# Kernel optimization log

Hardware: AMD Instinct MI355X
Metric: run time of the kernel (lower is better)

Reference implementation:

```python
import jax, jax.numpy as jnp
import numpy as np

# DeepSeek-style MLA decode paged attention (vLLM HPU flat_pa_mla, latent cache path)
B = 32              # batch (decode requests)
H = 16              # q heads (TP shard)
KV_LORA = 512       # kv_lora_rank
ROPE = 64           # qk_rope_head_dim
D = KV_LORA + ROPE  # 576, latent+rope dim
BS = 128            # block_size
BLOCKS_PER_SEQ = 16 # 2048-token context
NB = B * BLOCKS_PER_SEQ   # 512 active blocks
NCACHE = 1024       # blocks in the paged cache
SCALE = 192 ** -0.5  # 1/sqrt(qk_nope(128)+rope(64))
NEG = -1.0e9


def setup_inputs() -> dict:
    key = jax.random.key(0)
    k1, k2, k3, k4 = jax.random.split(key, 4)
    query = jax.random.normal(k1, (B, H, D), dtype=jnp.float32)
    key_cache = jax.random.normal(k2, (NCACHE, BS, D), dtype=jnp.float32)
    # each active block points at some cache block
    block_list = jax.random.randint(k3, (NB,), 0, NCACHE, dtype=jnp.int32)
    # contiguous grouping: blocks_per_seq blocks per request
    block_groups = jnp.repeat(jnp.arange(B, dtype=jnp.int32), BLOCKS_PER_SEQ)
    block_mapping = jax.nn.one_hot(block_groups, B, dtype=jnp.float32)  # [NB, B]
    # per-block usage in [1, BS]; unused tail positions masked out
    usage = jax.random.randint(k4, (NB,), 1, BS + 1)
    block_bias = jnp.where(jnp.arange(BS)[None, :] < usage[:, None], 0.0, NEG).astype(jnp.float32)
    return {"query": query, "key_cache": key_cache, "block_mapping": block_mapping,
            "block_bias": block_bias, "block_list": block_list, "block_groups": block_groups}


def reference(query, key_cache, block_mapping, block_bias, block_list, block_groups):
    # batch2block: scatter per-batch query to its blocks via one-hot matmul
    q = SCALE * jnp.einsum('nb,bhd->nhd', block_mapping, query)      # [NB,H,D]
    kv = key_cache[block_list]                                       # [NB,BS,D] fetched latent KV
    v = kv[..., :KV_LORA]                                            # [NB,BS,V]
    attn = jnp.einsum('nhd,nsd->nhs', q, kv) + block_bias[:, None, :]  # [NB,H,BS]
    # per-block online softmax pieces
    block_max = attn.max(axis=-1, keepdims=True)                     # [NB,H,1]
    p = jnp.exp(attn - block_max)
    block_sums = p.sum(axis=-1)                                      # [NB,H]
    o = jnp.einsum('nhs,nsv->nhv', p, v)                             # [NB,H,V]
    bm = block_max[..., 0]                                           # [NB,H]
    # grouped max over blocks of the same request, broadcast back to blocks
    group_max = jax.ops.segment_max(bm, block_groups, num_segments=B)[block_groups]
    adj = jnp.exp(bm - group_max)                                    # [NB,H]
    sum_adj = block_sums * adj
    # block2batch then batch2block of the adjusted sums
    group_sum = jnp.einsum('nb,nh->bh', block_mapping, sum_adj)
    group_sum = jnp.einsum('nb,bh->nh', block_mapping, group_sum)
    group_sum = jnp.maximum(group_sum, sum_adj)
    rescale = adj / group_sum
    o = o * rescale[..., None]
    # block2batch: sum rescaled partial outputs per request
    out = jnp.einsum('nb,nhv->bhv', block_mapping, o)                # [B,H,V]
    return out
```

## Files before the change

### kernel.cpp

```cpp
#include <hip/hip_runtime.h>
#include <math.h>

#define NB_ 512
#define B_ 32
#define H_ 16
#define D_ 576
#define KV_ 512
#define BS_ 128
#define SCALE_ 0.07216878364870323f

typedef __attribute__((ext_vector_type(8))) short bf16x8;
typedef __attribute__((ext_vector_type(4))) float f32x4;

__device__ float g_o[NB_ * H_ * KV_];
__device__ float g_bm[NB_ * H_];
__device__ float g_bs[NB_ * H_];

typedef const __attribute__((address_space(1))) void* gp_t;
typedef __attribute__((address_space(3))) void* lp_t;
typedef __attribute__((address_space(3))) char* l3p;

static __device__ __forceinline__ void glds16(const float* g, l3p l) {
    __builtin_amdgcn_global_load_lds((gp_t)g, (lp_t)l, 16, 0, 0);
}

static __device__ __forceinline__ unsigned int cvtpk(float a, float b) {
    unsigned int r;
    asm("v_cvt_pk_bf16_f32 %0, %1, %2" : "=v"(r) : "v"(a), "v"(b));
    return r;
}

static __device__ __forceinline__ bf16x8 pack8(float4 a, float4 b) {
    union { unsigned int u[4]; bf16x8 v; } r;
    r.u[0] = cvtpk(a.x, a.y);
    r.u[1] = cvtpk(a.z, a.w);
    r.u[2] = cvtpk(b.x, b.y);
    r.u[3] = cvtpk(b.z, b.w);
    return r.v;
}

__global__ __launch_bounds__(256, 2) void mla_block_kernel(
    const float* __restrict__ query,
    const float* __restrict__ key_cache,
    const float* __restrict__ block_bias,
    const int* __restrict__ block_list,
    const int* __restrict__ block_groups)
{
    __shared__ __align__(16) float smem[18560];
    float* p_s  = smem + 16384;
    float* mred = smem + 18432;
    float* lred = smem + 18496;

    const l3p lbase = (l3p)smem;
    const float* bufp[2] = { smem, smem + 8192 };

    const int tid = threadIdx.x;
    const int n   = blockIdx.x;
    const int b   = block_groups[n];
    const float* K = key_cache + (long)block_list[n] * (BS_ * D_);
    const float* Q = query + (long)b * (H_ * D_);

    const int w    = tid >> 6;
    const int lane = tid & 63;
    const int a15  = lane & 15;
    const int q4   = lane >> 4;
    const int krow = lane >> 4;
    const int kgc  = lane & 15;

    const float* bias = block_bias + n * BS_;
    const float b0 = bias[32 * w + a15];
    const float b1 = bias[32 * w + 16 + a15];

#pragma unroll
    for (int j = 0; j < 8; ++j) {
        int row = w * 32 + j * 4 + krow;
        glds16(K + row * D_ + 4 * (kgc ^ (row & 7)),
               lbase + (w * 32 + j * 4) * 256);
    }

    bf16x8 af[9][2];
#pragma unroll
    for (int kk = 0; kk < 9; ++kk)
#pragma unroll
        for (int t = 0; t < 2; ++t) {
            const float* qp = Q + a15 * D_ + kk * 64 + t * 32 + 8 * q4;
            float4 qa = *(const float4*)qp;
            float4 qb = *(const float4*)(qp + 4);
            af[kk][t] = pack8(qa, qb);
        }

    f32x4 acc0 = {0.f, 0.f, 0.f, 0.f};
    f32x4 acc1 = {0.f, 0.f, 0.f, 0.f};
    const int s0  = 32 * w + a15;
    const int key = a15 & 7;

#pragma unroll
    for (int kk = 0; kk < 9; ++kk) {
        __syncthreads();
        if (kk < 8) {
#pragma unroll
            for (int j = 0; j < 8; ++j) {
                int row = w * 32 + j * 4 + krow;
                glds16(K + row * D_ + (kk + 1) * 64 + 4 * (kgc ^ (row & 7)),
                       lbase + ((kk + 1) & 1) * 32768 + (w * 32 + j * 4) * 256);
            }
        } else {
#pragma unroll
            for (int j = 0; j < 8; ++j) {
                int fl = (w * 8 + j) * 64 + lane;
                glds16(K + (fl >> 7) * D_ + 4 * (fl & 127),
                       lbase + 32768 + (w * 8 + j) * 1024);
            }
        }
        const float* bk = bufp[kk & 1];
#pragma unroll
        for (int t = 0; t < 2; ++t) {
            int g0 = t * 8 + 2 * q4;
            float4 a0 = *(const float4*)(bk + s0 * 64        + 4 * ((g0    ) ^ key));
            float4 a1 = *(const float4*)(bk + s0 * 64        + 4 * ((g0 + 1) ^ key));
            float4 c0 = *(const float4*)(bk + (s0 + 16) * 64 + 4 * ((g0    ) ^ key));
            float4 c1 = *(const float4*)(bk + (s0 + 16) * 64 + 4 * ((g0 + 1) ^ key));
            acc0 = __builtin_amdgcn_mfma_f32_16x16x32_bf16(af[kk][t], pack8(a0, a1), acc0, 0, 0, 0);
            acc1 = __builtin_amdgcn_mfma_f32_16x16x32_bf16(af[kk][t], pack8(c0, c1), acc1, 0, 0, 0);
        }
    }

    float lg0[4], lg1[4], mw[4];
#pragma unroll
    for (int r = 0; r < 4; ++r) {
        lg0[r] = SCALE_ * acc0[r] + b0;
        lg1[r] = SCALE_ * acc1[r] + b1;
        float m = fmaxf(lg0[r], lg1[r]);
#pragma unroll
        for (int off = 1; off < 16; off <<= 1) m = fmaxf(m, __shfl_xor(m, off));
        mw[r] = m;
    }
    if (a15 == 0) {
#pragma unroll
        for (int r = 0; r < 4; ++r) mred[w * 16 + 4 * q4 + r] = mw[r];
    }
    __syncthreads();
    float mg[4], lw[4];
#pragma unroll
    for (int r = 0; r < 4; ++r) {
        int h = 4 * q4 + r;
        float m = fmaxf(fmaxf(mred[h], mred[16 + h]), fmaxf(mred[32 + h], mred[48 + h]));
        mg[r] = m;
        float p0 = __expf(lg0[r] - m);
        float p1 = __expf(lg1[r] - m);
        p_s[h * BS_ + 32 * w + a15]      = p0;
        p_s[h * BS_ + 32 * w + 16 + a15] = p1;
        float s = p0 + p1;
#pragma unroll
        for (int off = 1; off < 16; off <<= 1) s += __shfl_xor(s, off);
        lw[r] = s;
    }
    if (a15 == 0) {
#pragma unroll
        for (int r = 0; r < 4; ++r) lred[w * 16 + 4 * q4 + r] = lw[r];
    }
    __syncthreads();
    if (w == 0 && a15 == 0) {
#pragma unroll
        for (int r = 0; r < 4; ++r) {
            int h = 4 * q4 + r;
            g_bm[n * H_ + h] = mg[r];
            g_bs[n * H_ + h] = lred[h] + lred[16 + h] + lred[32 + h] + lred[48 + h];
        }
    }

    const int hg = w;
    const int sl = lane;
    float4 oa0[4], oa1[4];
#pragma unroll
    for (int i = 0; i < 4; ++i) {
        oa0[i] = make_float4(0.f, 0.f, 0.f, 0.f);
        oa1[i] = make_float4(0.f, 0.f, 0.f, 0.f);
    }
#pragma unroll
    for (int sc = 0; sc < 8; ++sc) {
        __syncthreads();
        if (sc < 7) {
#pragma unroll
            for (int j = 0; j < 8; ++j) {
                int fl = (w * 8 + j) * 64 + lane;
                glds16(K + (long)(16 * (sc + 1) + (fl >> 7)) * D_ + 4 * (fl & 127),
                       lbase + (sc & 1) * 32768 + (w * 8 + j) * 1024);
            }
        }
        const float* bv = bufp[(sc + 1) & 1];
#pragma unroll
        for (int sg = 0; sg < 4; ++sg) {
            float4 pv[4];
#pragma unroll
            for (int i = 0; i < 4; ++i)
                pv[i] = *(const float4*)(p_s + (4 * hg + i) * BS_ + 16 * sc + 4 * sg);
#pragma unroll
            for (int ss = 0; ss < 4; ++ss) {
                const int s = 4 * sg + ss;
                float4 v0 = *(const float4*)(bv + s * KV_ + 4 * sl);
                float4 v1 = *(const float4*)(bv + s * KV_ + 256 + 4 * sl);
#pragma unroll
                for (int i = 0; i < 4; ++i) {
                    const float p = ss == 0 ? pv[i].x : ss == 1 ? pv[i].y
                                  : ss == 2 ? pv[i].z : pv[i].w;
                    oa0[i].x += p * v0.x; oa0[i].y += p * v0.y;
                    oa0[i].z += p * v0.z; oa0[i].w += p * v0.w;
                    oa1[i].x += p * v1.x; oa1[i].y += p * v1.y;
                    oa1[i].z += p * v1.z; oa1[i].w += p * v1.w;
                }
            }
        }
    }

    float* op = g_o + (long)n * H_ * KV_;
#pragma unroll
    for (int i = 0; i < 4; ++i) {
        *(float4*)(op + (4 * hg + i) * KV_ + 4 * sl)       = oa0[i];
        *(float4*)(op + (4 * hg + i) * KV_ + 256 + 4 * sl) = oa1[i];
    }
}

__global__ __launch_bounds__(128) void mla_combine_kernel(float* __restrict__ out)
{
    const int gid  = blockIdx.x;
    const int bh   = gid >> 1;
    const int half = gid & 1;
    const int b = bh >> 4;
    const int h = bh & 15;
    const int tid = threadIdx.x;
    const int c4 = tid & 63;
    const int jh = tid >> 6;

    float bm[16];
    float m = -1e30f;
#pragma unroll
    for (int j = 0; j < 16; ++j) {
        bm[j] = g_bm[(16 * b + j) * H_ + h];
        m = fmaxf(m, bm[j]);
    }
    float sa[16];
    float gs = 0.f;
#pragma unroll
    for (int j = 0; j < 16; ++j) {
        sa[j] = g_bs[(16 * b + j) * H_ + h] * __expf(bm[j] - m);
        gs += sa[j];
    }

    float4 acc = make_float4(0.f, 0.f, 0.f, 0.f);
    if (jh == 0) {
#pragma unroll
        for (int j = 0; j < 8; ++j) {
            float r = __expf(bm[j] - m) / fmaxf(gs, sa[j]);
            const float4 v = *(const float4*)(g_o + ((long)((16 * b + j) * H_ + h)) * KV_
                                              + half * 256 + 4 * c4);
            acc.x += r * v.x; acc.y += r * v.y; acc.z += r * v.z; acc.w += r * v.w;
        }
    } else {
#pragma unroll
        for (int j = 8; j < 16; ++j) {
            float r = __expf(bm[j] - m) / fmaxf(gs, sa[j]);
            const float4 v = *(const float4*)(g_o + ((long)((16 * b + j) * H_ + h)) * KV_
                                              + half * 256 + 4 * c4);
            acc.x += r * v.x; acc.y += r * v.y; acc.z += r * v.z; acc.w += r * v.w;
        }
    }
    __shared__ float4 red[64];
    if (jh) red[c4] = acc;
    __syncthreads();
    if (!jh) {
        float4 o2 = red[c4];
        acc.x += o2.x; acc.y += o2.y; acc.z += o2.z; acc.w += o2.w;
        *(float4*)(out + (long)bh * KV_ + half * 256 + 4 * c4) = acc;
    }
}

extern "C" void kernel_launch(void* const* d_in, const int* in_sizes, int n_in,
                              void* d_out, int out_size, void* d_ws, size_t ws_size,
                              hipStream_t stream)
{
    const float* query        = (const float*)d_in[0];
    const float* key_cache    = (const float*)d_in[1];
    const float* block_bias   = (const float*)d_in[3];
    const int*   block_list   = (const int*)d_in[4];
    const int*   block_groups = (const int*)d_in[5];
    float* out = (float*)d_out;

    mla_block_kernel<<<NB_, 256, 0, stream>>>(query, key_cache, block_bias,
                                              block_list, block_groups);
    mla_combine_kernel<<<B_ * H_ * 2, 128, 0, stream>>>(out);
}
```

Before: 462.6 us.

## Drop LDS double-buffered K/V staging, load operands directly from global

Removes the global_load_lds double-buffered staging of the key/value block through shared memory. The QK MFMA operands and the PV value rows are now read straight from global memory into registers. This gets rid of the per-chunk barriers and about 64KB of LDS, which could allow more resident workgroups. In exchange the loads are no longer prefetched ahead of use, and the four waves each re-read the same V rows from global or L2 instead of sharing them through LDS.

```diff
diff --git a/kernel.cpp b/kernel.cpp
--- a/kernel.cpp
+++ b/kernel.cpp
@@ -16,14 +16,6 @@
 __device__ float g_bm[NB_ * H_];
 __device__ float g_bs[NB_ * H_];
 
-typedef const __attribute__((address_space(1))) void* gp_t;
-typedef __attribute__((address_space(3))) void* lp_t;
-typedef __attribute__((address_space(3))) char* l3p;
-
-static __device__ __forceinline__ void glds16(const float* g, l3p l) {
-    __builtin_amdgcn_global_load_lds((gp_t)g, (lp_t)l, 16, 0, 0);
-}
-
 static __device__ __forceinline__ unsigned int cvtpk(float a, float b) {
     unsigned int r;
     asm("v_cvt_pk_bf16_f32 %0, %1, %2" : "=v"(r) : "v"(a), "v"(b));
@@ -46,13 +38,9 @@
     const int* __restrict__ block_list,
     const int* __restrict__ block_groups)
 {
-    __shared__ __align__(16) float smem[18560];
-    float* p_s  = smem + 16384;
-    float* mred = smem + 18432;
-    float* lred = smem + 18496;
-
-    const l3p lbase = (l3p)smem;
-    const float* bufp[2] = { smem, smem + 8192 };
+    __shared__ __align__(16) float p_s[H_ * BS_];
+    __shared__ float mred[64];
+    __shared__ float lred[64];
 
     const int tid = threadIdx.x;
     const int n   = blockIdx.x;
@@ -64,64 +52,33 @@
     const int lane = tid & 63;
     const int a15  = lane & 15;
     const int q4   = lane >> 4;
-    const int krow = lane >> 4;
-    const int kgc  = lane & 15;
 
     const float* bias = block_bias + n * BS_;
     const float b0 = bias[32 * w + a15];
     const float b1 = bias[32 * w + 16 + a15];
 
-#pragma unroll
-    for (int j = 0; j < 8; ++j) {
-        int row = w * 32 + j * 4 + krow;
-        glds16(K + row * D_ + 4 * (kgc ^ (row & 7)),
-               lbase + (w * 32 + j * 4) * 256);
-    }
-
-    bf16x8 af[9][2];
-#pragma unroll
-    for (int kk = 0; kk < 9; ++kk)
-#pragma unroll
-        for (int t = 0; t < 2; ++t) {
-            const float* qp = Q + a15 * D_ + kk * 64 + t * 32 + 8 * q4;
-            float4 qa = *(const float4*)qp;
-            float4 qb = *(const float4*)(qp + 4);
-            af[kk][t] = pack8(qa, qb);
-        }
+    const float* Qf  = Q + a15 * D_ + 8 * q4;
+    const float* Kf0 = K + (32 * w + a15) * D_ + 8 * q4;
+    const float* Kf1 = Kf0 + 16 * D_;
 
     f32x4 acc0 = {0.f, 0.f, 0.f, 0.f};
     f32x4 acc1 = {0.f, 0.f, 0.f, 0.f};
-    const int s0  = 32 * w + a15;
-    const int key = a15 & 7;
-
 #pragma unroll
     for (int kk = 0; kk < 9; ++kk) {
-        __syncthreads();
-        if (kk < 8) {
-#pragma unroll
-            for (int j = 0; j < 8; ++j) {
-                int row = w * 32 + j * 4 + krow;
-                glds16(K + row * D_ + (kk + 1) * 64 + 4 * (kgc ^ (row & 7)),
-                       lbase + ((kk + 1) & 1) * 32768 + (w * 32 + j * 4) * 256);
-            }
-        } else {
-#pragma unroll
-            for (int j = 0; j < 8; ++j) {
-                int fl = (w * 8 + j) * 64 + lane;
-                glds16(K + (fl >> 7) * D_ + 4 * (fl & 127),
-                       lbase + 32768 + (w * 8 + j) * 1024);
-            }
-        }
-        const float* bk = bufp[kk & 1];
 #pragma unroll
         for (int t = 0; t < 2; ++t) {
-            int g0 = t * 8 + 2 * q4;
-            float4 a0 = *(const float4*)(bk + s0 * 64        + 4 * ((g0    ) ^ key));
-            float4 a1 = *(const float4*)(bk + s0 * 64        + 4 * ((g0 + 1) ^ key));
-            float4 c0 = *(const float4*)(bk + (s0 + 16) * 64 + 4 * ((g0    ) ^ key));
-            float4 c1 = *(const float4*)(bk + (s0 + 16) * 64 + 4 * ((g0 + 1) ^ key));
-            acc0 = __builtin_amdgcn_mfma_f32_16x16x32_bf16(af[kk][t], pack8(a0, a1), acc0, 0, 0, 0);
-            acc1 = __builtin_amdgcn_mfma_f32_16x16x32_bf16(af[kk][t], pack8(c0, c1), acc1, 0, 0, 0);
+            const int off = kk * 64 + t * 32;
+            float4 qa = *(const float4*)(Qf  + off);
+            float4 qb = *(const float4*)(Qf  + off + 4);
+            float4 k0a = *(const float4*)(Kf0 + off);
+            float4 k0b = *(const float4*)(Kf0 + off + 4);
+            float4 k1a = *(const float4*)(Kf1 + off);
+            float4 k1b = *(const float4*)(Kf1 + off + 4);
+            bf16x8 a  = pack8(qa, qb);
+            bf16x8 f0 = pack8(k0a, k0b);
+            bf16x8 f1 = pack8(k1a, k1b);
+            acc0 = __builtin_amdgcn_mfma_f32_16x16x32_bf16(a, f0, acc0, 0, 0, 0);
+            acc1 = __builtin_amdgcn_mfma_f32_16x16x32_bf16(a, f1, acc1, 0, 0, 0);
         }
     }
 
@@ -177,38 +134,26 @@
         oa0[i] = make_float4(0.f, 0.f, 0.f, 0.f);
         oa1[i] = make_float4(0.f, 0.f, 0.f, 0.f);
     }
-#pragma unroll
-    for (int sc = 0; sc < 8; ++sc) {
-        __syncthreads();
-        if (sc < 7) {
-#pragma unroll
-            for (int j = 0; j < 8; ++j) {
-                int fl = (w * 8 + j) * 64 + lane;
-                glds16(K + (long)(16 * (sc + 1) + (fl >> 7)) * D_ + 4 * (fl & 127),
-                       lbase + (sc & 1) * 32768 + (w * 8 + j) * 1024);
-            }
-        }
-        const float* bv = bufp[(sc + 1) & 1];
-#pragma unroll
-        for (int sg = 0; sg < 4; ++sg) {
-            float4 pv[4];
-#pragma unroll
-            for (int i = 0; i < 4; ++i)
-                pv[i] = *(const float4*)(p_s + (4 * hg + i) * BS_ + 16 * sc + 4 * sg);
-#pragma unroll
-            for (int ss = 0; ss < 4; ++ss) {
-                const int s = 4 * sg + ss;
-                float4 v0 = *(const float4*)(bv + s * KV_ + 4 * sl);
-                float4 v1 = *(const float4*)(bv + s * KV_ + 256 + 4 * sl);
-#pragma unroll
-                for (int i = 0; i < 4; ++i) {
-                    const float p = ss == 0 ? pv[i].x : ss == 1 ? pv[i].y
-                                  : ss == 2 ? pv[i].z : pv[i].w;
-                    oa0[i].x += p * v0.x; oa0[i].y += p * v0.y;
-                    oa0[i].z += p * v0.z; oa0[i].w += p * v0.w;
-                    oa1[i].x += p * v1.x; oa1[i].y += p * v1.y;
-                    oa1[i].z += p * v1.z; oa1[i].w += p * v1.w;
-                }
+    const float* Vb = K + 4 * sl;
+#pragma unroll 4
+    for (int s4 = 0; s4 < 32; ++s4) {
+        float4 pv[4];
+#pragma unroll
+        for (int i = 0; i < 4; ++i)
+            pv[i] = *(const float4*)(p_s + (4 * hg + i) * BS_ + 4 * s4);
+#pragma unroll
+        for (int ss = 0; ss < 4; ++ss) {
+            const int s = 4 * s4 + ss;
+            float4 v0 = *(const float4*)(Vb + (long)s * D_);
+            float4 v1 = *(const float4*)(Vb + (long)s * D_ + 256);
+#pragma unroll
+            for (int i = 0; i < 4; ++i) {
+                const float p = ss == 0 ? pv[i].x : ss == 1 ? pv[i].y
+                              : ss == 2 ? pv[i].z : pv[i].w;
+                oa0[i].x += p * v0.x; oa0[i].y += p * v0.y;
+                oa0[i].z += p * v0.z; oa0[i].w += p * v0.w;
+                oa1[i].x += p * v1.x; oa1[i].y += p * v1.y;
+                oa1[i].z += p * v1.z; oa1[i].w += p * v1.w;
             }
         }
     }
```

Measured after the change: 411.6 us. 1.12x faster.
